# Optimization experiments

Hardware: AMD Instinct MI355X
Metric: run time of the kernel (lower is better)

## Reference

```python
import jax, jax.numpy as jnp
import numpy as np

B, S, H, R, F, E, K = 4, 2048, 1024, 256, 4096, 8, 2


def setup_inputs() -> dict:
    key = jax.random.key(0)
    k = jax.random.split(key, 7)
    s = 0.02
    return {
        "x": jax.random.normal(k[0], (B, S, H), dtype=jnp.float32),
        "router_w": jax.random.normal(k[1], (H, E), dtype=jnp.float32) * s,
        "router_b": jnp.zeros((E,), dtype=jnp.float32),
        "w1": jax.random.normal(k[2], (E, H, R), dtype=jnp.float32) * s,  # expert Linear(hidden->rank), no bias
        "w2": jax.random.normal(k[3], (E, R, F), dtype=jnp.float32) * s,  # expert Linear(rank->ffn), no bias
        "lin2_w": jax.random.normal(k[4], (F, H), dtype=jnp.float32) * s,
        "lin2_b": jnp.zeros((H,), dtype=jnp.float32),
    }


def reference(x, router_w, router_b, w1, w2, lin2_w, lin2_b):
    # Router: softmax over experts, top-k selection (mask), weight by softmax prob
    logits = jnp.einsum("bsh,he->bse", x, router_w) + router_b
    routing_weights = jax.nn.softmax(logits, axis=-1)            # [B,S,E]
    _, topk_idx = jax.lax.top_k(routing_weights, K)              # [B,S,K]
    mask = jnp.sum(jax.nn.one_hot(topk_idx, E, dtype=x.dtype), axis=-2)  # [B,S,E] in {0,1}
    mw = routing_weights * mask                                  # mask * weight per expert

    # Dense per-expert low-rank FFN (original computes all experts, masks after).
    # Fold mask*weight into the rank-space activations to avoid a [B,S,E,F] tensor.
    t = jnp.einsum("bsh,ehr->bser", x, w1)                       # [B,S,E,R]
    t = t * mw[..., None]
    mixed = jnp.einsum("bser,erf->bsf", t, w2)                   # [B,S,F]

    h = jax.nn.gelu(mixed, approximate=False)                    # torch nn.GELU is erf-based
    out = jnp.einsum("bsf,fh->bsh", h, lin2_w) + lin2_b
    # dropout is identity in eval mode
    return out
```

## Files before the change

kernel.cpp:

```cpp
#include <hip/hip_runtime.h>
#include <math.h>


using short8  = __attribute__((ext_vector_type(8))) short;
using floatx4 = __attribute__((ext_vector_type(4))) float;
typedef unsigned short bf16_t;

#define TOK   8192
#define HDIM  1024
#define RDIM  256
#define FDIM  4096
#define NEXP  8
#define MAXTILES 96
#define MAXSLOTS 16384

__device__ __forceinline__ bf16_t f2bf(float f) {
  union { float f; unsigned u; } a; a.f = f;
  unsigned u = a.u;
  return (bf16_t)((u + 0x7FFFu + ((u >> 16) & 1u)) >> 16);
}

__device__ __forceinline__ float gelu_erf(float v) {
  return 0.5f * v * (1.0f + erff(v * 0.70710678118654752f));
}

__device__ __forceinline__ void gload16(const void* g, void* l) {
  __builtin_amdgcn_global_load_lds(
      (const __attribute__((address_space(1))) void*)g,
      (__attribute__((address_space(3))) void*)l, 16, 0, 0);
}


__global__ void tcvt(const float* __restrict__ in, bf16_t* __restrict__ out,
                     int cols, size_t inSlice, size_t ldo,
                     int outRowStep, int outColStep) {
  __shared__ float tile[64][65];
  const int z  = blockIdx.z;
  const float* src = in + (size_t)z * inSlice;
  const int c0 = blockIdx.x * 64;
  const int r0 = blockIdx.y * 64;
  const int tx = threadIdx.x;
  const int ty = threadIdx.y;
#pragma unroll
  for (int i = 0; i < 64; i += 4)
    tile[ty + i][tx] = src[(size_t)(r0 + ty + i) * cols + (c0 + tx)];
  __syncthreads();
#pragma unroll
  for (int i = 0; i < 64; i += 4) {
    float v = tile[tx][ty + i];
    out[((size_t)(c0 + ty + i) + (size_t)z * outRowStep) * ldo +
        (size_t)z * outColStep + (r0 + tx)] = f2bf(v);
  }
}


__global__ void router_kernel(const float* __restrict__ x,
                              const float* __restrict__ rw,
                              const float* __restrict__ rb,
                              int* __restrict__ gid_tok,
                              float2* __restrict__ tokscale,
                              bf16_t* __restrict__ xb) {
  const int token = blockIdx.x * 4 + (threadIdx.x >> 6);
  const int lane  = threadIdx.x & 63;
  const float* xr = x + (size_t)token * HDIM;
  bf16_t* xbr = xb + (size_t)token * HDIM;

  double acc[NEXP];
#pragma unroll
  for (int e = 0; e < NEXP; e++) acc[e] = 0.0;
  for (int h = lane; h < HDIM; h += 64) {
    const float xf = xr[h];
    xbr[h] = f2bf(xf);
    const double xv = (double)xf;
    const float* wr = rw + (size_t)h * NEXP;
#pragma unroll
    for (int e = 0; e < NEXP; e++) acc[e] += xv * (double)wr[e];
  }
#pragma unroll
  for (int off = 32; off > 0; off >>= 1) {
#pragma unroll
    for (int e = 0; e < NEXP; e++) acc[e] += __shfl_xor(acc[e], off, 64);
  }
  double lg[NEXP];
#pragma unroll
  for (int e = 0; e < NEXP; e++) lg[e] = acc[e] + (double)rb[e];

  double mx = lg[0];
#pragma unroll
  for (int e = 1; e < NEXP; e++) mx = fmax(mx, lg[e]);
  double p[NEXP]; double den = 0.0;
#pragma unroll
  for (int e = 0; e < NEXP; e++) { p[e] = exp(lg[e] - mx); den += p[e]; }

  int i1 = 0;
#pragma unroll
  for (int e = 1; e < NEXP; e++) if (lg[e] > lg[i1]) i1 = e;
  int i2 = (i1 == 0) ? 1 : 0;
#pragma unroll
  for (int e = 0; e < NEXP; e++)
    if (e != i1 && e != i2 && lg[e] > lg[i2]) i2 = e;

  if (lane == 0) {
    const int elo = min(i1, i2), ehi = max(i1, i2);
    gid_tok[token] = elo * 8 + ehi;
    tokscale[token] = make_float2((float)(p[elo] / den), (float)(p[ehi] / den));
  }
}

__global__ void build_tiles(const int* __restrict__ gid_tok,
                            int* __restrict__ ctrl,
                            int* __restrict__ tok_of_slot,
                            float2* __restrict__ scale_of_slot) {
  __shared__ int hist[64], ntl[64];
  const int t = threadIdx.x;
  for (int i = t; i < MAXSLOTS; i += 256) {
    tok_of_slot[i] = -1;
    scale_of_slot[i] = make_float2(0.f, 0.f);
  }
  if (t < 64) { hist[t] = 0; }
  __syncthreads();
  for (int i = t; i < TOK; i += 256) atomicAdd(&hist[gid_tok[i]], 1);
  __syncthreads();
  if (t < 64) ntl[t] = (hist[t] + 127) >> 7;
  __syncthreads();
  if (t < 64) {
    int slot0 = 0, tile0 = 0;
    for (int g = 0; g < t; g++) { slot0 += ntl[g] << 7; tile0 += ntl[g]; }
    ctrl[64 + t] = 0;
    ctrl[128 + t] = slot0;
    const int nt = ntl[t], c = hist[t];
    for (int i = 0; i < nt; i++) {
      ctrl[256 + (tile0 + i) * 3 + 0] = t;
      ctrl[256 + (tile0 + i) * 3 + 1] = slot0 + i * 128;
      ctrl[256 + (tile0 + i) * 3 + 2] = min(128, c - i * 128);
    }
    if (t == 63) ctrl[192] = tile0 + nt;
  }
}

__global__ void scatter_tokens(const int* __restrict__ gid_tok,
                               const float2* __restrict__ tokscale,
                               int* __restrict__ ctrl,
                               int* __restrict__ tok_of_slot,
                               float2* __restrict__ scale_of_slot) {
  const int t = blockIdx.x * 256 + threadIdx.x;
  const int g = gid_tok[t];
  const int pos = atomicAdd(&ctrl[64 + g], 1);
  const int slot = ctrl[128 + g] + pos;
  tok_of_slot[slot] = t;
  scale_of_slot[slot] = tokscale[t];
}


__global__ __launch_bounds__(256)
void gemm_g1(const bf16_t* __restrict__ xb, const bf16_t* __restrict__ w1t,
             bf16_t* __restrict__ Tp, const int* __restrict__ ctrl,
             const int* __restrict__ tok_of_slot,
             const float2* __restrict__ scale_of_slot) {
  const int b = blockIdx.x;
  const int tile = b % MAXTILES, nt = b / MAXTILES;
  if (tile >= ctrl[192]) return;
  __shared__ bf16_t As[128 * 64];
  __shared__ bf16_t Bs[64 * 64];
  const int gid   = ctrl[256 + tile * 3];
  const int slot0 = ctrl[256 + tile * 3 + 1];
  const int e = (nt < 4) ? (gid >> 3) : (gid & 7);
  const int tid = threadIdx.x, lane = tid & 63, w = tid >> 6;
  const int l16 = lane & 15, quad = lane >> 4;
  const int rl = lane >> 3, gg = lane & 7;
  const int gf = (gg ^ rl) * 8;

  floatx4 acc[2][4];
  const floatx4 zero = {0.f, 0.f, 0.f, 0.f};
#pragma unroll
  for (int i = 0; i < 2; i++)
#pragma unroll
    for (int j = 0; j < 4; j++) acc[i][j] = zero;

  const bf16_t* ga[4];
#pragma unroll
  for (int c = 0; c < 4; c++) {
    int tk = tok_of_slot[slot0 + w * 32 + c * 8 + rl];
    if (tk < 0) tk = 0;
    ga[c] = xb + (size_t)tk * HDIM + gf;
  }
  const bf16_t* gb[2];
#pragma unroll
  for (int c = 0; c < 2; c++)
    gb[c] = w1t + (size_t)(e * 256 + (nt & 3) * 64 + w * 16 + c * 8 + rl) * HDIM + gf;
  bf16_t* lA = &As[w * 32 * 64];
  bf16_t* lB = &Bs[w * 16 * 64];

  for (int k0 = 0; k0 < HDIM; k0 += 64) {
    __syncthreads();
#pragma unroll
    for (int c = 0; c < 4; c++) { gload16(ga[c], lA + c * 512); ga[c] += 64; }
#pragma unroll
    for (int c = 0; c < 2; c++) { gload16(gb[c], lB + c * 512); gb[c] += 64; }
    __syncthreads();
#pragma unroll
    for (int s = 0; s < 2; s++) {
      const int pg = ((s * 4 + quad) ^ (l16 & 7)) * 8;
      short8 af[2], bfr[4];
#pragma unroll
      for (int i = 0; i < 2; i++)
        af[i] = *(const short8*)&As[(w * 32 + i * 16 + l16) * 64 + pg];
#pragma unroll
      for (int i = 0; i < 4; i++)
        bfr[i] = *(const short8*)&Bs[(i * 16 + l16) * 64 + pg];
#pragma unroll
      for (int mi = 0; mi < 2; mi++)
#pragma unroll
        for (int ni = 0; ni < 4; ni++)
          acc[mi][ni] = __builtin_amdgcn_mfma_f32_16x16x32_bf16(
              af[mi], bfr[ni], acc[mi][ni], 0, 0, 0);
    }
  }

#pragma unroll
  for (int mi = 0; mi < 2; mi++) {
#pragma unroll
    for (int r = 0; r < 4; r++) {
      const int srow = slot0 + w * 32 + mi * 16 + quad * 4 + r;
      const float2 sc = scale_of_slot[srow];
      const float s = (nt < 4) ? sc.x : sc.y;
#pragma unroll
      for (int ni = 0; ni < 4; ni++) {
        const int col = nt * 64 + ni * 16 + l16;
        Tp[(size_t)srow * 512 + col] = f2bf(acc[mi][ni][r] * s);
      }
    }
  }
}

__global__ __launch_bounds__(256)
void gemm_g2(const bf16_t* __restrict__ Tp, const bf16_t* __restrict__ w2t,
             bf16_t* __restrict__ Hb, const int* __restrict__ ctrl,
             const int* __restrict__ tok_of_slot) {
  const int b = blockIdx.x;
  const int tile = b % MAXTILES, n = b / MAXTILES;
  if (tile >= ctrl[192]) return;
  __shared__ bf16_t As[128 * 64];
  __shared__ bf16_t Bs[128 * 64];
  const int gid   = ctrl[256 + tile * 3];
  const int slot0 = ctrl[256 + tile * 3 + 1];
  const int n0 = n * 128;
  const int elo = gid >> 3, ehi = gid & 7;
  const int tid = threadIdx.x, lane = tid & 63, w = tid >> 6;
  const int wm = (w >> 1) * 64, wn = (w & 1) * 64;
  const int l16 = lane & 15, quad = lane >> 4;
  const int rl = lane >> 3, gg = lane & 7;
  const int gf = (gg ^ rl) * 8;

  floatx4 acc[4][4];
  const floatx4 zero = {0.f, 0.f, 0.f, 0.f};
#pragma unroll
  for (int i = 0; i < 4; i++)
#pragma unroll
    for (int j = 0; j < 4; j++) acc[i][j] = zero;

  const bf16_t* ga[4];
  const bf16_t* gbr[4];
#pragma unroll
  for (int c = 0; c < 4; c++) {
    ga[c]  = Tp + (size_t)(slot0 + w * 32 + c * 8 + rl) * 512 + gf;
    gbr[c] = w2t + (size_t)(n0 + w * 32 + c * 8 + rl) * 2048 + gf;
  }
  bf16_t* lA = &As[w * 32 * 64];
  bf16_t* lB = &Bs[w * 32 * 64];

#pragma unroll
  for (int t = 0; t < 8; t++) {
    const int e = (t < 4) ? elo : ehi;
    const int bcol = e * 256 + (t & 3) * 64;
    __syncthreads();
#pragma unroll
    for (int c = 0; c < 4; c++) { gload16(ga[c], lA + c * 512); ga[c] += 64; }
#pragma unroll
    for (int c = 0; c < 4; c++) gload16(gbr[c] + bcol, lB + c * 512);
    __syncthreads();
#pragma unroll
    for (int s = 0; s < 2; s++) {
      const int pg = ((s * 4 + quad) ^ (l16 & 7)) * 8;
      short8 af[4], bfr[4];
#pragma unroll
      for (int i = 0; i < 4; i++)
        af[i] = *(const short8*)&As[(wm + i * 16 + l16) * 64 + pg];
#pragma unroll
      for (int i = 0; i < 4; i++)
        bfr[i] = *(const short8*)&Bs[(wn + i * 16 + l16) * 64 + pg];
#pragma unroll
      for (int mi = 0; mi < 4; mi++)
#pragma unroll
        for (int ni = 0; ni < 4; ni++)
          acc[mi][ni] = __builtin_amdgcn_mfma_f32_16x16x32_bf16(
              af[mi], bfr[ni], acc[mi][ni], 0, 0, 0);
    }
  }

#pragma unroll
  for (int mi = 0; mi < 4; mi++) {
#pragma unroll
    for (int r = 0; r < 4; r++) {
      const int srow = slot0 + wm + mi * 16 + quad * 4 + r;
      const int tok = tok_of_slot[srow];
      if (tok < 0) continue;
#pragma unroll
      for (int ni = 0; ni < 4; ni++) {
        const int col = n0 + wn + ni * 16 + l16;
        Hb[(size_t)tok * FDIM + col] = f2bf(gelu_erf(acc[mi][ni][r]));
      }
    }
  }
}

__global__ __launch_bounds__(256)
void gemm_g3(const bf16_t* __restrict__ Hb, const bf16_t* __restrict__ ltw,
             float* __restrict__ out, const float* __restrict__ bias) {
  __shared__ bf16_t As[128 * 64];
  __shared__ bf16_t Bs[128 * 64];
  const int b = blockIdx.x;
  const int m0 = ((b & 7) * 8 + ((b >> 3) & 7)) * 128;
  const int n0 = (b >> 6) * 128;
  const int tid = threadIdx.x, lane = tid & 63, w = tid >> 6;
  const int wm = (w >> 1) * 64, wn = (w & 1) * 64;
  const int l16 = lane & 15, quad = lane >> 4;
  const int rl = lane >> 3, gg = lane & 7;
  const int gf = (gg ^ rl) * 8;

  floatx4 acc[4][4];
  const floatx4 zero = {0.f, 0.f, 0.f, 0.f};
#pragma unroll
  for (int i = 0; i < 4; i++)
#pragma unroll
    for (int j = 0; j < 4; j++) acc[i][j] = zero;

  const bf16_t* ga[4];
  const bf16_t* gb[4];
#pragma unroll
  for (int c = 0; c < 4; c++) {
    ga[c] = Hb  + (size_t)(m0 + w * 32 + c * 8 + rl) * FDIM + gf;
    gb[c] = ltw + (size_t)(n0 + w * 32 + c * 8 + rl) * FDIM + gf;
  }
  bf16_t* lA = &As[w * 32 * 64];
  bf16_t* lB = &Bs[w * 32 * 64];

  for (int k0 = 0; k0 < FDIM; k0 += 64) {
    __syncthreads();
#pragma unroll
    for (int c = 0; c < 4; c++) { gload16(ga[c], lA + c * 512); ga[c] += 64; }
#pragma unroll
    for (int c = 0; c < 4; c++) { gload16(gb[c], lB + c * 512); gb[c] += 64; }
    __syncthreads();
#pragma unroll
    for (int s = 0; s < 2; s++) {
      const int pg = ((s * 4 + quad) ^ (l16 & 7)) * 8;
      short8 af[4], bfr[4];
#pragma unroll
      for (int i = 0; i < 4; i++)
        af[i] = *(const short8*)&As[(wm + i * 16 + l16) * 64 + pg];
#pragma unroll
      for (int i = 0; i < 4; i++)
        bfr[i] = *(const short8*)&Bs[(wn + i * 16 + l16) * 64 + pg];
#pragma unroll
      for (int mi = 0; mi < 4; mi++)
#pragma unroll
        for (int ni = 0; ni < 4; ni++)
          acc[mi][ni] = __builtin_amdgcn_mfma_f32_16x16x32_bf16(
              af[mi], bfr[ni], acc[mi][ni], 0, 0, 0);
    }
  }

#pragma unroll
  for (int mi = 0; mi < 4; mi++) {
#pragma unroll
    for (int ni = 0; ni < 4; ni++) {
      const int row = m0 + wm + mi * 16 + quad * 4;
      const int col = n0 + wn + ni * 16 + l16;
#pragma unroll
      for (int r = 0; r < 4; r++)
        out[(size_t)(row + r) * HDIM + col] = acc[mi][ni][r] + bias[col];
    }
  }
}


extern "C" void kernel_launch(void* const* d_in, const int* in_sizes, int n_in,
                              void* d_out, int out_size, void* d_ws, size_t ws_size,
                              hipStream_t stream) {
  const float* x   = (const float*)d_in[0];
  const float* rw  = (const float*)d_in[1];
  const float* rb  = (const float*)d_in[2];
  const float* w1  = (const float*)d_in[3];
  const float* w2  = (const float*)d_in[4];
  const float* l2w = (const float*)d_in[5];
  const float* l2b = (const float*)d_in[6];

  char* ws = (char*)d_ws;
  int*    ctrl     = (int*)   (ws + 0);
  int*    gid_tok  = (int*)   (ws + 4096);
  float2* tokscale = (float2*)(ws + 36864);
  int*    tokslot  = (int*)   (ws + 102400);
  float2* slotsc   = (float2*)(ws + 167936);
  bf16_t* xb  = (bf16_t*)(ws + 1048576);
  bf16_t* w1t = (bf16_t*)(ws + 17825792);
  bf16_t* w2t = (bf16_t*)(ws + 22020096);
  bf16_t* ltw = (bf16_t*)(ws + 38797312);
  bf16_t* Tp  = (bf16_t*)(ws + 47185920);
  bf16_t* Hb  = (bf16_t*)(ws + 63963136);

  router_kernel<<<TOK / 4, 256, 0, stream>>>(x, rw, rb, gid_tok, tokscale, xb);
  build_tiles<<<1, 256, 0, stream>>>(gid_tok, ctrl, tokslot, slotsc);
  scatter_tokens<<<TOK / 256, 256, 0, stream>>>(gid_tok, tokscale, ctrl, tokslot, slotsc);

  tcvt<<<dim3(RDIM / 64, HDIM / 64, NEXP), dim3(64, 4), 0, stream>>>(
      w1, w1t, RDIM, (size_t)HDIM * RDIM, HDIM, RDIM, 0);
  tcvt<<<dim3(FDIM / 64, RDIM / 64, NEXP), dim3(64, 4), 0, stream>>>(
      w2, w2t, FDIM, (size_t)RDIM * FDIM, 2048, 0, RDIM);
  tcvt<<<dim3(HDIM / 64, FDIM / 64, 1), dim3(64, 4), 0, stream>>>(
      l2w, ltw, HDIM, 0, FDIM, 0, 0);

  gemm_g1<<<8 * MAXTILES, 256, 0, stream>>>(xb, w1t, Tp, ctrl, tokslot, slotsc);
  gemm_g2<<<32 * MAXTILES, 256, 0, stream>>>(Tp, w2t, Hb, ctrl, tokslot);
  gemm_g3<<<512, 256, 0, stream>>>(Hb, ltw, (float*)d_out, l2b);
}
```

Before: 366.2 us.

## Pre-pack operands into swizzled 128x128 bf16 tile images with K=128 stages

Replaces the transpose-convert kernels with pack kernels that write weights as contiguous, pre-swizzled 128x128 bf16 tile images. The intermediate activations (Tp, Hb) are also written directly in this tiled image layout. All three GEMMs then load whole tiles with fully contiguous 16-byte global-to-LDS copies and use K=128 per stage, halving the barrier count. gemm_g1 moves to 128x128 output tiles with fewer blocks. The cost is doubled LDS per block (64 KB), which may lower occupancy, plus more complex scattered epilogue writes into the tiled images.

```diff
diff --git a/kernel.cpp b/kernel.cpp
--- a/kernel.cpp
+++ b/kernel.cpp
@@ -13,6 +13,7 @@
 #define NEXP  8
 #define MAXTILES 96
 #define MAXSLOTS 16384
+#define IMG   16384
 
 __device__ __forceinline__ bf16_t f2bf(float f) {
   union { float f; unsigned u; } a; a.f = f;
@@ -30,27 +31,43 @@
       (__attribute__((address_space(3))) void*)l, 16, 0, 0);
 }
 
-
-__global__ void tcvt(const float* __restrict__ in, bf16_t* __restrict__ out,
-                     int cols, size_t inSlice, size_t ldo,
-                     int outRowStep, int outColStep) {
-  __shared__ float tile[64][65];
-  const int z  = blockIdx.z;
-  const float* src = in + (size_t)z * inSlice;
-  const int c0 = blockIdx.x * 64;
-  const int r0 = blockIdx.y * 64;
-  const int tx = threadIdx.x;
-  const int ty = threadIdx.y;
-#pragma unroll
-  for (int i = 0; i < 64; i += 4)
-    tile[ty + i][tx] = src[(size_t)(r0 + ty + i) * cols + (c0 + tx)];
+__device__ __forceinline__ int swz_off(int r, int kl) {
+  return r * 128 + ((((kl >> 3) ^ (r & 15)) << 3) | (kl & 7));
+}
+
+
+__device__ __forceinline__ void pack_tile_body(const float* __restrict__ src,
+                                               size_t kStride,
+                                               bf16_t* __restrict__ img) {
+  __shared__ bf16_t lim[IMG];
+  const int tid = threadIdx.x;
+  const int rr = tid & 127, half = tid >> 7;
+  for (int kl = half; kl < 128; kl += 2)
+    lim[swz_off(rr, kl)] = f2bf(src[(size_t)kl * kStride + rr]);
   __syncthreads();
-#pragma unroll
-  for (int i = 0; i < 64; i += 4) {
-    float v = tile[tx][ty + i];
-    out[((size_t)(c0 + ty + i) + (size_t)z * outRowStep) * ldo +
-        (size_t)z * outColStep + (r0 + tx)] = f2bf(v);
-  }
+  const int4* s4 = (const int4*)lim;
+  int4* d4 = (int4*)img;
+#pragma unroll
+  for (int i = 0; i < 8; i++) d4[tid + i * 256] = s4[tid + i * 256];
+}
+
+__global__ void pack_w1(const float* __restrict__ w1, bf16_t* __restrict__ w1p) {
+  const int img = blockIdx.x;
+  const int e = img >> 4, nc = (img >> 3) & 1, kb = img & 7;
+  pack_tile_body(w1 + (size_t)e * 1024 * 256 + (size_t)kb * 128 * 256 + nc * 128,
+                 256, w1p + (size_t)img * IMG);
+}
+__global__ void pack_w2(const float* __restrict__ w2, bf16_t* __restrict__ w2p) {
+  const int img = blockIdx.x;
+  const int n = img >> 4, e = (img >> 1) & 7, kb = img & 1;
+  pack_tile_body(w2 + (size_t)e * 256 * 4096 + (size_t)kb * 128 * 4096 + n * 128,
+                 4096, w2p + (size_t)img * IMG);
+}
+__global__ void pack_ltw(const float* __restrict__ l2w, bf16_t* __restrict__ ltwp) {
+  const int img = blockIdx.x;
+  const int n = img >> 5, kb = img & 31;
+  pack_tile_body(l2w + (size_t)kb * 128 * 1024 + n * 128, 1024,
+                 ltwp + (size_t)img * IMG);
 }
 
 
@@ -117,7 +134,7 @@
     tok_of_slot[i] = -1;
     scale_of_slot[i] = make_float2(0.f, 0.f);
   }
-  if (t < 64) { hist[t] = 0; }
+  if (t < 64) hist[t] = 0;
   __syncthreads();
   for (int i = t; i < TOK; i += 256) atomicAdd(&hist[gid_tok[i]], 1);
   __syncthreads();
@@ -153,63 +170,60 @@
 
 
 __global__ __launch_bounds__(256)
-void gemm_g1(const bf16_t* __restrict__ xb, const bf16_t* __restrict__ w1t,
+void gemm_g1(const bf16_t* __restrict__ xb, const bf16_t* __restrict__ w1p,
              bf16_t* __restrict__ Tp, const int* __restrict__ ctrl,
              const int* __restrict__ tok_of_slot,
              const float2* __restrict__ scale_of_slot) {
   const int b = blockIdx.x;
-  const int tile = b % MAXTILES, nt = b / MAXTILES;
+  const int tile = b >> 2, nt = b & 3;
   if (tile >= ctrl[192]) return;
-  __shared__ bf16_t As[128 * 64];
-  __shared__ bf16_t Bs[64 * 64];
+  __shared__ bf16_t As[IMG];
+  __shared__ bf16_t Bs[IMG];
   const int gid   = ctrl[256 + tile * 3];
   const int slot0 = ctrl[256 + tile * 3 + 1];
-  const int e = (nt < 4) ? (gid >> 3) : (gid & 7);
+  const int e = (nt < 2) ? (gid >> 3) : (gid & 7);
+  const int nc = nt & 1;
   const int tid = threadIdx.x, lane = tid & 63, w = tid >> 6;
+  const int wm = (w >> 1) * 64, wn = (w & 1) * 64;
   const int l16 = lane & 15, quad = lane >> 4;
-  const int rl = lane >> 3, gg = lane & 7;
-  const int gf = (gg ^ rl) * 8;
-
-  floatx4 acc[2][4];
+
+  floatx4 acc[4][4];
   const floatx4 zero = {0.f, 0.f, 0.f, 0.f};
 #pragma unroll
-  for (int i = 0; i < 2; i++)
+  for (int i = 0; i < 4; i++)
 #pragma unroll
     for (int j = 0; j < 4; j++) acc[i][j] = zero;
 
-  const bf16_t* ga[4];
-#pragma unroll
-  for (int c = 0; c < 4; c++) {
-    int tk = tok_of_slot[slot0 + w * 32 + c * 8 + rl];
-    if (tk < 0) tk = 0;
-    ga[c] = xb + (size_t)tk * HDIM + gf;
-  }
-  const bf16_t* gb[2];
-#pragma unroll
-  for (int c = 0; c < 2; c++)
-    gb[c] = w1t + (size_t)(e * 256 + (nt & 3) * 64 + w * 16 + c * 8 + rl) * HDIM + gf;
-  bf16_t* lA = &As[w * 32 * 64];
-  bf16_t* lB = &Bs[w * 16 * 64];
-
-  for (int k0 = 0; k0 < HDIM; k0 += 64) {
-    __syncthreads();
-#pragma unroll
-    for (int c = 0; c < 4; c++) { gload16(ga[c], lA + c * 512); ga[c] += 64; }
-#pragma unroll
-    for (int c = 0; c < 2; c++) { gload16(gb[c], lB + c * 512); gb[c] += 64; }
-    __syncthreads();
-#pragma unroll
-    for (int s = 0; s < 2; s++) {
-      const int pg = ((s * 4 + quad) ^ (l16 & 7)) * 8;
-      short8 af[2], bfr[4];
-#pragma unroll
-      for (int i = 0; i < 2; i++)
-        af[i] = *(const short8*)&As[(w * 32 + i * 16 + l16) * 64 + pg];
-#pragma unroll
-      for (int i = 0; i < 4; i++)
-        bfr[i] = *(const short8*)&Bs[(i * 16 + l16) * 64 + pg];
-#pragma unroll
-      for (int mi = 0; mi < 2; mi++)
+  int toks[8];
+#pragma unroll
+  for (int i = 0; i < 8; i++) {
+    int tk = tok_of_slot[slot0 + w * 32 + i * 4 + (lane >> 4)];
+    toks[i] = (tk < 0) ? 0 : tk;
+  }
+  const bf16_t* bimg = w1p + (size_t)(e * 16 + nc * 8) * IMG;
+  bf16_t* lA = As + w * 4096;
+  bf16_t* lB = Bs + w * 4096;
+
+  for (int kb = 0; kb < 8; kb++) {
+    __syncthreads();
+#pragma unroll
+    for (int i = 0; i < 8; i++) {
+      const int g = (lane & 15) ^ ((i * 4 + (lane >> 4)) & 15);
+      gload16(xb + (size_t)toks[i] * HDIM + kb * 128 + g * 8, lA + i * 512);
+      gload16(bimg + (size_t)kb * IMG + w * 4096 + i * 512 + lane * 8, lB + i * 512);
+    }
+    __syncthreads();
+#pragma unroll
+    for (int s = 0; s < 4; s++) {
+      const int pg = ((s * 4 + quad) ^ l16) << 3;
+      short8 af[4], bfr[4];
+#pragma unroll
+      for (int i = 0; i < 4; i++) {
+        af[i]  = *(const short8*)&As[(wm + i * 16 + l16) * 128 + pg];
+        bfr[i] = *(const short8*)&Bs[(wn + i * 16 + l16) * 128 + pg];
+      }
+#pragma unroll
+      for (int mi = 0; mi < 4; mi++)
 #pragma unroll
         for (int ni = 0; ni < 4; ni++)
           acc[mi][ni] = __builtin_amdgcn_mfma_f32_16x16x32_bf16(
@@ -217,40 +231,38 @@
     }
   }
 
-#pragma unroll
-  for (int mi = 0; mi < 2; mi++) {
+  bf16_t* img = Tp + (size_t)(tile * 4 + nt) * IMG;
+#pragma unroll
+  for (int mi = 0; mi < 4; mi++) {
 #pragma unroll
     for (int r = 0; r < 4; r++) {
-      const int srow = slot0 + w * 32 + mi * 16 + quad * 4 + r;
-      const float2 sc = scale_of_slot[srow];
-      const float s = (nt < 4) ? sc.x : sc.y;
+      const int rl = wm + mi * 16 + quad * 4 + r;
+      const float2 sc = scale_of_slot[slot0 + rl];
+      const float s = (nt < 2) ? sc.x : sc.y;
 #pragma unroll
       for (int ni = 0; ni < 4; ni++) {
-        const int col = nt * 64 + ni * 16 + l16;
-        Tp[(size_t)srow * 512 + col] = f2bf(acc[mi][ni][r] * s);
+        const int c = wn + ni * 16 + l16;
+        img[swz_off(rl, c)] = f2bf(acc[mi][ni][r] * s);
       }
     }
   }
 }
 
 __global__ __launch_bounds__(256)
-void gemm_g2(const bf16_t* __restrict__ Tp, const bf16_t* __restrict__ w2t,
-             bf16_t* __restrict__ Hb, const int* __restrict__ ctrl,
+void gemm_g2(const bf16_t* __restrict__ Tp, const bf16_t* __restrict__ w2p,
+             bf16_t* __restrict__ Hbp, const int* __restrict__ ctrl,
              const int* __restrict__ tok_of_slot) {
   const int b = blockIdx.x;
-  const int tile = b % MAXTILES, n = b / MAXTILES;
+  const int tile = b >> 5, n = b & 31;
   if (tile >= ctrl[192]) return;
-  __shared__ bf16_t As[128 * 64];
-  __shared__ bf16_t Bs[128 * 64];
+  __shared__ bf16_t As[IMG];
+  __shared__ bf16_t Bs[IMG];
   const int gid   = ctrl[256 + tile * 3];
   const int slot0 = ctrl[256 + tile * 3 + 1];
-  const int n0 = n * 128;
   const int elo = gid >> 3, ehi = gid & 7;
   const int tid = threadIdx.x, lane = tid & 63, w = tid >> 6;
   const int wm = (w >> 1) * 64, wn = (w & 1) * 64;
   const int l16 = lane & 15, quad = lane >> 4;
-  const int rl = lane >> 3, gg = lane & 7;
-  const int gf = (gg ^ rl) * 8;
 
   floatx4 acc[4][4];
   const floatx4 zero = {0.f, 0.f, 0.f, 0.f};
@@ -259,36 +271,30 @@
 #pragma unroll
     for (int j = 0; j < 4; j++) acc[i][j] = zero;
 
-  const bf16_t* ga[4];
-  const bf16_t* gbr[4];
-#pragma unroll
-  for (int c = 0; c < 4; c++) {
-    ga[c]  = Tp + (size_t)(slot0 + w * 32 + c * 8 + rl) * 512 + gf;
-    gbr[c] = w2t + (size_t)(n0 + w * 32 + c * 8 + rl) * 2048 + gf;
-  }
-  bf16_t* lA = &As[w * 32 * 64];
-  bf16_t* lB = &Bs[w * 32 * 64];
-
-#pragma unroll
-  for (int t = 0; t < 8; t++) {
-    const int e = (t < 4) ? elo : ehi;
-    const int bcol = e * 256 + (t & 3) * 64;
-    __syncthreads();
-#pragma unroll
-    for (int c = 0; c < 4; c++) { gload16(ga[c], lA + c * 512); ga[c] += 64; }
-#pragma unroll
-    for (int c = 0; c < 4; c++) gload16(gbr[c] + bcol, lB + c * 512);
-    __syncthreads();
-#pragma unroll
-    for (int s = 0; s < 2; s++) {
-      const int pg = ((s * 4 + quad) ^ (l16 & 7)) * 8;
+  const bf16_t* aimg = Tp + (size_t)tile * 4 * IMG;
+  bf16_t* lA = As + w * 4096;
+  bf16_t* lB = Bs + w * 4096;
+
+#pragma unroll
+  for (int t = 0; t < 4; t++) {
+    const int e = (t < 2) ? elo : ehi;
+    const bf16_t* bimg = w2p + (size_t)(n * 16 + e * 2 + (t & 1)) * IMG;
+    __syncthreads();
+#pragma unroll
+    for (int i = 0; i < 8; i++) {
+      gload16(aimg + (size_t)t * IMG + w * 4096 + i * 512 + lane * 8, lA + i * 512);
+      gload16(bimg + w * 4096 + i * 512 + lane * 8, lB + i * 512);
+    }
+    __syncthreads();
+#pragma unroll
+    for (int s = 0; s < 4; s++) {
+      const int pg = ((s * 4 + quad) ^ l16) << 3;
       short8 af[4], bfr[4];
 #pragma unroll
-      for (int i = 0; i < 4; i++)
-        af[i] = *(const short8*)&As[(wm + i * 16 + l16) * 64 + pg];
-#pragma unroll
-      for (int i = 0; i < 4; i++)
-        bfr[i] = *(const short8*)&Bs[(wn + i * 16 + l16) * 64 + pg];
+      for (int i = 0; i < 4; i++) {
+        af[i]  = *(const short8*)&As[(wm + i * 16 + l16) * 128 + pg];
+        bfr[i] = *(const short8*)&Bs[(wn + i * 16 + l16) * 128 + pg];
+      }
 #pragma unroll
       for (int mi = 0; mi < 4; mi++)
 #pragma unroll
@@ -305,28 +311,28 @@
       const int srow = slot0 + wm + mi * 16 + quad * 4 + r;
       const int tok = tok_of_slot[srow];
       if (tok < 0) continue;
+      bf16_t* img = Hbp + (size_t)((tok >> 7) * 32 + n) * IMG;
+      const int rloc = tok & 127;
 #pragma unroll
       for (int ni = 0; ni < 4; ni++) {
-        const int col = n0 + wn + ni * 16 + l16;
-        Hb[(size_t)tok * FDIM + col] = f2bf(gelu_erf(acc[mi][ni][r]));
+        const int kl = wn + ni * 16 + l16;
+        img[swz_off(rloc, kl)] = f2bf(gelu_erf(acc[mi][ni][r]));
       }
     }
   }
 }
 
 __global__ __launch_bounds__(256)
-void gemm_g3(const bf16_t* __restrict__ Hb, const bf16_t* __restrict__ ltw,
+void gemm_g3(const bf16_t* __restrict__ Hbp, const bf16_t* __restrict__ ltwp,
              float* __restrict__ out, const float* __restrict__ bias) {
-  __shared__ bf16_t As[128 * 64];
-  __shared__ bf16_t Bs[128 * 64];
+  __shared__ bf16_t As[IMG];
+  __shared__ bf16_t Bs[IMG];
   const int b = blockIdx.x;
-  const int m0 = ((b & 7) * 8 + ((b >> 3) & 7)) * 128;
-  const int n0 = (b >> 6) * 128;
+  const int mtile = (b & 7) * 8 + ((b >> 3) & 7);
+  const int n = b >> 6;
   const int tid = threadIdx.x, lane = tid & 63, w = tid >> 6;
   const int wm = (w >> 1) * 64, wn = (w & 1) * 64;
   const int l16 = lane & 15, quad = lane >> 4;
-  const int rl = lane >> 3, gg = lane & 7;
-  const int gf = (gg ^ rl) * 8;
 
   floatx4 acc[4][4];
   const floatx4 zero = {0.f, 0.f, 0.f, 0.f};
@@ -335,33 +341,28 @@
 #pragma unroll
     for (int j = 0; j < 4; j++) acc[i][j] = zero;
 
-  const bf16_t* ga[4];
-  const bf16_t* gb[4];
-#pragma unroll
-  for (int c = 0; c < 4; c++) {
-    ga[c] = Hb  + (size_t)(m0 + w * 32 + c * 8 + rl) * FDIM + gf;
-    gb[c] = ltw + (size_t)(n0 + w * 32 + c * 8 + rl) * FDIM + gf;
-  }
-  bf16_t* lA = &As[w * 32 * 64];
-  bf16_t* lB = &Bs[w * 32 * 64];
-
-  for (int k0 = 0; k0 < FDIM; k0 += 64) {
-    __syncthreads();
-#pragma unroll
-    for (int c = 0; c < 4; c++) { gload16(ga[c], lA + c * 512); ga[c] += 64; }
-#pragma unroll
-    for (int c = 0; c < 4; c++) { gload16(gb[c], lB + c * 512); gb[c] += 64; }
-    __syncthreads();
-#pragma unroll
-    for (int s = 0; s < 2; s++) {
-      const int pg = ((s * 4 + quad) ^ (l16 & 7)) * 8;
+  const bf16_t* aimg = Hbp + (size_t)mtile * 32 * IMG;
+  const bf16_t* bimg = ltwp + (size_t)n * 32 * IMG;
+  bf16_t* lA = As + w * 4096;
+  bf16_t* lB = Bs + w * 4096;
+
+  for (int kb = 0; kb < 32; kb++) {
+    __syncthreads();
+#pragma unroll
+    for (int i = 0; i < 8; i++) {
+      gload16(aimg + (size_t)kb * IMG + w * 4096 + i * 512 + lane * 8, lA + i * 512);
+      gload16(bimg + (size_t)kb * IMG + w * 4096 + i * 512 + lane * 8, lB + i * 512);
+    }
+    __syncthreads();
+#pragma unroll
+    for (int s = 0; s < 4; s++) {
+      const int pg = ((s * 4 + quad) ^ l16) << 3;
       short8 af[4], bfr[4];
 #pragma unroll
-      for (int i = 0; i < 4; i++)
-        af[i] = *(const short8*)&As[(wm + i * 16 + l16) * 64 + pg];
-#pragma unroll
-      for (int i = 0; i < 4; i++)
-        bfr[i] = *(const short8*)&Bs[(wn + i * 16 + l16) * 64 + pg];
+      for (int i = 0; i < 4; i++) {
+        af[i]  = *(const short8*)&As[(wm + i * 16 + l16) * 128 + pg];
+        bfr[i] = *(const short8*)&Bs[(wn + i * 16 + l16) * 128 + pg];
+      }
 #pragma unroll
       for (int mi = 0; mi < 4; mi++)
 #pragma unroll
@@ -375,8 +376,8 @@
   for (int mi = 0; mi < 4; mi++) {
 #pragma unroll
     for (int ni = 0; ni < 4; ni++) {
-      const int row = m0 + wm + mi * 16 + quad * 4;
-      const int col = n0 + wn + ni * 16 + l16;
+      const int row = mtile * 128 + wm + mi * 16 + quad * 4;
+      const int col = n * 128 + wn + ni * 16 + l16;
 #pragma unroll
       for (int r = 0; r < 4; r++)
         out[(size_t)(row + r) * HDIM + col] = acc[mi][ni][r] + bias[col];
@@ -402,25 +403,22 @@
   float2* tokscale = (float2*)(ws + 36864);
   int*    tokslot  = (int*)   (ws + 102400);
   float2* slotsc   = (float2*)(ws + 167936);
-  bf16_t* xb  = (bf16_t*)(ws + 1048576);
-  bf16_t* w1t = (bf16_t*)(ws + 17825792);
-  bf16_t* w2t = (bf16_t*)(ws + 22020096);
-  bf16_t* ltw = (bf16_t*)(ws + 38797312);
-  bf16_t* Tp  = (bf16_t*)(ws + 47185920);
-  bf16_t* Hb  = (bf16_t*)(ws + 63963136);
+  bf16_t* xb   = (bf16_t*)(ws + 1048576);
+  bf16_t* w1p  = (bf16_t*)(ws + 17825792);
+  bf16_t* w2p  = (bf16_t*)(ws + 22020096);
+  bf16_t* ltwp = (bf16_t*)(ws + 38797312);
+  bf16_t* Tp   = (bf16_t*)(ws + 47185920);
+  bf16_t* Hbp  = (bf16_t*)(ws + 59768832);
 
   router_kernel<<<TOK / 4, 256, 0, stream>>>(x, rw, rb, gid_tok, tokscale, xb);
   build_tiles<<<1, 256, 0, stream>>>(gid_tok, ctrl, tokslot, slotsc);
   scatter_tokens<<<TOK / 256, 256, 0, stream>>>(gid_tok, tokscale, ctrl, tokslot, slotsc);
 
-  tcvt<<<dim3(RDIM / 64, HDIM / 64, NEXP), dim3(64, 4), 0, stream>>>(
-      w1, w1t, RDIM, (size_t)HDIM * RDIM, HDIM, RDIM, 0);
-  tcvt<<<dim3(FDIM / 64, RDIM / 64, NEXP), dim3(64, 4), 0, stream>>>(
-      w2, w2t, FDIM, (size_t)RDIM * FDIM, 2048, 0, RDIM);
-  tcvt<<<dim3(HDIM / 64, FDIM / 64, 1), dim3(64, 4), 0, stream>>>(
-      l2w, ltw, HDIM, 0, FDIM, 0, 0);
-
-  gemm_g1<<<8 * MAXTILES, 256, 0, stream>>>(xb, w1t, Tp, ctrl, tokslot, slotsc);
-  gemm_g2<<<32 * MAXTILES, 256, 0, stream>>>(Tp, w2t, Hb, ctrl, tokslot);
-  gemm_g3<<<512, 256, 0, stream>>>(Hb, ltw, (float*)d_out, l2b);
-}
+  pack_w1<<<128, 256, 0, stream>>>(w1, w1p);
+  pack_w2<<<512, 256, 0, stream>>>(w2, w2p);
+  pack_ltw<<<256, 256, 0, stream>>>(l2w, ltwp);
+
+  gemm_g1<<<4 * MAXTILES, 256, 0, stream>>>(xb, w1p, Tp, ctrl, tokslot, slotsc);
+  gemm_g2<<<32 * MAXTILES, 256, 0, stream>>>(Tp, w2p, Hbp, ctrl, tokslot);
+  gemm_g3<<<512, 256, 0, stream>>>(Hbp, ltwp, (float*)d_out, l2b);
+}
```

Result: slower. 375.6 us (+2.5%).

## Pre-pack expert weights into swizzled tile images and restructure expert GEMMs

Applied to the files above, without the earlier changes.

Replaces the w1/w2 transpose-convert with pack kernels that write each 128x128 bf16 weight block as a pre-swizzled contiguous image, so the grouped GEMMs can stream B tiles with plain linear loads. gemm_g1 and gemm_g2 now use 64-row M halves with K=128 steps, skip the second half when a tile holds 64 rows or fewer, and stage outputs through LDS. g1 writes the intermediate in the same tiled image layout for g2, and g2 writes full 16-byte rows into the scattered token positions. The risks are doubled block counts for g2, extra LDS traffic in the epilogue, and less reuse per block from the smaller M tiles.

```diff
diff --git a/kernel.cpp b/kernel.cpp
--- a/kernel.cpp
+++ b/kernel.cpp
@@ -13,6 +13,7 @@
 #define NEXP  8
 #define MAXTILES 96
 #define MAXSLOTS 16384
+#define IMG   16384
 
 __device__ __forceinline__ bf16_t f2bf(float f) {
   union { float f; unsigned u; } a; a.f = f;
@@ -30,6 +31,38 @@
       (__attribute__((address_space(3))) void*)l, 16, 0, 0);
 }
 
+__device__ __forceinline__ int swz_off(int r, int kl) {
+  return r * 128 + ((((kl >> 3) ^ (r & 15)) << 3) | (kl & 7));
+}
+
+
+__device__ __forceinline__ void pack_tile_body(const float* __restrict__ src,
+                                               size_t kStride,
+                                               bf16_t* __restrict__ img) {
+  __shared__ bf16_t lim[IMG];
+  const int tid = threadIdx.x;
+  const int rr = tid & 127, half = tid >> 7;
+  for (int kl = half; kl < 128; kl += 2)
+    lim[swz_off(rr, kl)] = f2bf(src[(size_t)kl * kStride + rr]);
+  __syncthreads();
+  const int4* s4 = (const int4*)lim;
+  int4* d4 = (int4*)img;
+#pragma unroll
+  for (int i = 0; i < 8; i++) d4[tid + i * 256] = s4[tid + i * 256];
+}
+
+__global__ void pack_w1(const float* __restrict__ w1, bf16_t* __restrict__ w1p) {
+  const int img = blockIdx.x;
+  const int e = img >> 4, nc = (img >> 3) & 1, kb = img & 7;
+  pack_tile_body(w1 + (size_t)e * 1024 * 256 + (size_t)kb * 128 * 256 + nc * 128,
+                 256, w1p + (size_t)img * IMG);
+}
+__global__ void pack_w2(const float* __restrict__ w2, bf16_t* __restrict__ w2p) {
+  const int img = blockIdx.x;
+  const int n = img >> 4, e = (img >> 1) & 7, kb = img & 1;
+  pack_tile_body(w2 + (size_t)e * 256 * 4096 + (size_t)kb * 128 * 4096 + n * 128,
+                 4096, w2p + (size_t)img * IMG);
+}
 
 __global__ void tcvt(const float* __restrict__ in, bf16_t* __restrict__ out,
                      int cols, size_t inSlice, size_t ldo,
@@ -117,7 +150,7 @@
     tok_of_slot[i] = -1;
     scale_of_slot[i] = make_float2(0.f, 0.f);
   }
-  if (t < 64) { hist[t] = 0; }
+  if (t < 64) hist[t] = 0;
   __syncthreads();
   for (int i = t; i < TOK; i += 256) atomicAdd(&hist[gid_tok[i]], 1);
   __syncthreads();
@@ -151,24 +184,25 @@
   scale_of_slot[slot] = tokscale[t];
 }
 
-
 __global__ __launch_bounds__(256)
-void gemm_g1(const bf16_t* __restrict__ xb, const bf16_t* __restrict__ w1t,
+void gemm_g1(const bf16_t* __restrict__ xb, const bf16_t* __restrict__ w1p,
              bf16_t* __restrict__ Tp, const int* __restrict__ ctrl,
              const int* __restrict__ tok_of_slot,
              const float2* __restrict__ scale_of_slot) {
   const int b = blockIdx.x;
-  const int tile = b % MAXTILES, nt = b / MAXTILES;
+  const int tile = b >> 3, mh = (b >> 2) & 1, n = b & 3;
   if (tile >= ctrl[192]) return;
-  __shared__ bf16_t As[128 * 64];
-  __shared__ bf16_t Bs[64 * 64];
+  const int nrows = ctrl[256 + tile * 3 + 2];
+  if (mh && nrows <= 64) return;
+  __shared__ bf16_t As[64 * 128];
+  __shared__ bf16_t Bs[128 * 128];
   const int gid   = ctrl[256 + tile * 3];
   const int slot0 = ctrl[256 + tile * 3 + 1];
-  const int e = (nt < 4) ? (gid >> 3) : (gid & 7);
+  const int e = (n < 2) ? (gid >> 3) : (gid & 7);
+  const int nc = n & 1;
   const int tid = threadIdx.x, lane = tid & 63, w = tid >> 6;
+  const int wm = (w & 1) * 32, wn = (w >> 1) * 64;
   const int l16 = lane & 15, quad = lane >> 4;
-  const int rl = lane >> 3, gg = lane & 7;
-  const int gf = (gg ^ rl) * 8;
 
   floatx4 acc[2][4];
   const floatx4 zero = {0.f, 0.f, 0.f, 0.f};
@@ -177,37 +211,39 @@
 #pragma unroll
     for (int j = 0; j < 4; j++) acc[i][j] = zero;
 
-  const bf16_t* ga[4];
-#pragma unroll
-  for (int c = 0; c < 4; c++) {
-    int tk = tok_of_slot[slot0 + w * 32 + c * 8 + rl];
-    if (tk < 0) tk = 0;
-    ga[c] = xb + (size_t)tk * HDIM + gf;
-  }
-  const bf16_t* gb[2];
-#pragma unroll
-  for (int c = 0; c < 2; c++)
-    gb[c] = w1t + (size_t)(e * 256 + (nt & 3) * 64 + w * 16 + c * 8 + rl) * HDIM + gf;
-  bf16_t* lA = &As[w * 32 * 64];
-  bf16_t* lB = &Bs[w * 16 * 64];
-
-  for (int k0 = 0; k0 < HDIM; k0 += 64) {
-    __syncthreads();
-#pragma unroll
-    for (int c = 0; c < 4; c++) { gload16(ga[c], lA + c * 512); ga[c] += 64; }
-#pragma unroll
-    for (int c = 0; c < 2; c++) { gload16(gb[c], lB + c * 512); gb[c] += 64; }
-    __syncthreads();
-#pragma unroll
-    for (int s = 0; s < 2; s++) {
-      const int pg = ((s * 4 + quad) ^ (l16 & 7)) * 8;
+  int toks[4];
+  int rowAs[4];
+#pragma unroll
+  for (int i = 0; i < 4; i++) {
+    rowAs[i] = w * 16 + i * 4 + (lane >> 4);
+    int tk = tok_of_slot[slot0 + mh * 64 + rowAs[i]];
+    toks[i] = (tk < 0) ? 0 : tk;
+  }
+  const bf16_t* bimg = w1p + (size_t)(e * 16 + nc * 8) * IMG;
+  bf16_t* lA = As + w * 2048;
+  bf16_t* lB = Bs + w * 4096;
+
+  for (int kb = 0; kb < 8; kb++) {
+    __syncthreads();
+#pragma unroll
+    for (int i = 0; i < 4; i++) {
+      const int gq = (lane & 15) ^ (rowAs[i] & 15);
+      gload16(xb + (size_t)toks[i] * HDIM + kb * 128 + gq * 8, lA + i * 512);
+    }
+#pragma unroll
+    for (int i = 0; i < 8; i++)
+      gload16(bimg + (size_t)kb * IMG + w * 4096 + i * 512 + lane * 8, lB + i * 512);
+    __syncthreads();
+#pragma unroll
+    for (int s = 0; s < 4; s++) {
+      const int pg = ((s * 4 + quad) ^ l16) << 3;
       short8 af[2], bfr[4];
 #pragma unroll
       for (int i = 0; i < 2; i++)
-        af[i] = *(const short8*)&As[(w * 32 + i * 16 + l16) * 64 + pg];
+        af[i] = *(const short8*)&As[(wm + i * 16 + l16) * 128 + pg];
 #pragma unroll
       for (int i = 0; i < 4; i++)
-        bfr[i] = *(const short8*)&Bs[(i * 16 + l16) * 64 + pg];
+        bfr[i] = *(const short8*)&Bs[(wn + i * 16 + l16) * 128 + pg];
 #pragma unroll
       for (int mi = 0; mi < 2; mi++)
 #pragma unroll
@@ -217,80 +253,82 @@
     }
   }
 
+  __syncthreads();
 #pragma unroll
   for (int mi = 0; mi < 2; mi++) {
 #pragma unroll
     for (int r = 0; r < 4; r++) {
-      const int srow = slot0 + w * 32 + mi * 16 + quad * 4 + r;
-      const float2 sc = scale_of_slot[srow];
-      const float s = (nt < 4) ? sc.x : sc.y;
+      const int rloc = wm + mi * 16 + quad * 4 + r;
+      const float2 sc = scale_of_slot[slot0 + mh * 64 + rloc];
+      const float s = (n < 2) ? sc.x : sc.y;
 #pragma unroll
       for (int ni = 0; ni < 4; ni++) {
-        const int col = nt * 64 + ni * 16 + l16;
-        Tp[(size_t)srow * 512 + col] = f2bf(acc[mi][ni][r] * s);
+        const int c = wn + ni * 16 + l16;
+        As[swz_off(rloc, c)] = f2bf(acc[mi][ni][r] * s);
       }
     }
   }
+  __syncthreads();
+  bf16_t* img = Tp + (size_t)(tile * 4 + n) * IMG + mh * 64 * 128;
+  const int4* s4 = (const int4*)As;
+  int4* d4 = (int4*)img;
+#pragma unroll
+  for (int j = 0; j < 4; j++) d4[tid + j * 256] = s4[tid + j * 256];
 }
 
 __global__ __launch_bounds__(256)
-void gemm_g2(const bf16_t* __restrict__ Tp, const bf16_t* __restrict__ w2t,
+void gemm_g2(const bf16_t* __restrict__ Tp, const bf16_t* __restrict__ w2p,
              bf16_t* __restrict__ Hb, const int* __restrict__ ctrl,
              const int* __restrict__ tok_of_slot) {
   const int b = blockIdx.x;
-  const int tile = b % MAXTILES, n = b / MAXTILES;
+  const int tile = b >> 6, mh = (b >> 5) & 1, n = b & 31;
   if (tile >= ctrl[192]) return;
-  __shared__ bf16_t As[128 * 64];
-  __shared__ bf16_t Bs[128 * 64];
+  const int nrows = ctrl[256 + tile * 3 + 2];
+  if (mh && nrows <= 64) return;
+  __shared__ bf16_t As[64 * 128];
+  __shared__ bf16_t Bs[128 * 128];
   const int gid   = ctrl[256 + tile * 3];
   const int slot0 = ctrl[256 + tile * 3 + 1];
-  const int n0 = n * 128;
   const int elo = gid >> 3, ehi = gid & 7;
   const int tid = threadIdx.x, lane = tid & 63, w = tid >> 6;
-  const int wm = (w >> 1) * 64, wn = (w & 1) * 64;
+  const int wm = (w & 1) * 32, wn = (w >> 1) * 64;
   const int l16 = lane & 15, quad = lane >> 4;
-  const int rl = lane >> 3, gg = lane & 7;
-  const int gf = (gg ^ rl) * 8;
-
-  floatx4 acc[4][4];
+
+  floatx4 acc[2][4];
   const floatx4 zero = {0.f, 0.f, 0.f, 0.f};
 #pragma unroll
-  for (int i = 0; i < 4; i++)
+  for (int i = 0; i < 2; i++)
 #pragma unroll
     for (int j = 0; j < 4; j++) acc[i][j] = zero;
 
-  const bf16_t* ga[4];
-  const bf16_t* gbr[4];
-#pragma unroll
-  for (int c = 0; c < 4; c++) {
-    ga[c]  = Tp + (size_t)(slot0 + w * 32 + c * 8 + rl) * 512 + gf;
-    gbr[c] = w2t + (size_t)(n0 + w * 32 + c * 8 + rl) * 2048 + gf;
-  }
-  bf16_t* lA = &As[w * 32 * 64];
-  bf16_t* lB = &Bs[w * 32 * 64];
-
-#pragma unroll
-  for (int t = 0; t < 8; t++) {
-    const int e = (t < 4) ? elo : ehi;
-    const int bcol = e * 256 + (t & 3) * 64;
-    __syncthreads();
-#pragma unroll
-    for (int c = 0; c < 4; c++) { gload16(ga[c], lA + c * 512); ga[c] += 64; }
-#pragma unroll
-    for (int c = 0; c < 4; c++) gload16(gbr[c] + bcol, lB + c * 512);
-    __syncthreads();
-#pragma unroll
-    for (int s = 0; s < 2; s++) {
-      const int pg = ((s * 4 + quad) ^ (l16 & 7)) * 8;
-      short8 af[4], bfr[4];
+  const bf16_t* aimg = Tp + (size_t)tile * 4 * IMG + mh * 64 * 128;
+  bf16_t* lA = As + w * 2048;
+  bf16_t* lB = Bs + w * 4096;
+
+#pragma unroll
+  for (int t = 0; t < 4; t++) {
+    const int e = (t < 2) ? elo : ehi;
+    const bf16_t* bimg = w2p + (size_t)(n * 16 + e * 2 + (t & 1)) * IMG;
+    __syncthreads();
+#pragma unroll
+    for (int i = 0; i < 4; i++)
+      gload16(aimg + (size_t)t * IMG + w * 2048 + i * 512 + lane * 8, lA + i * 512);
+#pragma unroll
+    for (int i = 0; i < 8; i++)
+      gload16(bimg + w * 4096 + i * 512 + lane * 8, lB + i * 512);
+    __syncthreads();
+#pragma unroll
+    for (int s = 0; s < 4; s++) {
+      const int pg = ((s * 4 + quad) ^ l16) << 3;
+      short8 af[2], bfr[4];
+#pragma unroll
+      for (int i = 0; i < 2; i++)
+        af[i] = *(const short8*)&As[(wm + i * 16 + l16) * 128 + pg];
 #pragma unroll
       for (int i = 0; i < 4; i++)
-        af[i] = *(const short8*)&As[(wm + i * 16 + l16) * 64 + pg];
-#pragma unroll
-      for (int i = 0; i < 4; i++)
-        bfr[i] = *(const short8*)&Bs[(wn + i * 16 + l16) * 64 + pg];
-#pragma unroll
-      for (int mi = 0; mi < 4; mi++)
+        bfr[i] = *(const short8*)&Bs[(wn + i * 16 + l16) * 128 + pg];
+#pragma unroll
+      for (int mi = 0; mi < 2; mi++)
 #pragma unroll
         for (int ni = 0; ni < 4; ni++)
           acc[mi][ni] = __builtin_amdgcn_mfma_f32_16x16x32_bf16(
@@ -298,19 +336,28 @@
     }
   }
 
-#pragma unroll
-  for (int mi = 0; mi < 4; mi++) {
+  __syncthreads();
+#pragma unroll
+  for (int mi = 0; mi < 2; mi++) {
 #pragma unroll
     for (int r = 0; r < 4; r++) {
-      const int srow = slot0 + wm + mi * 16 + quad * 4 + r;
-      const int tok = tok_of_slot[srow];
-      if (tok < 0) continue;
+      const int rloc = wm + mi * 16 + quad * 4 + r;
 #pragma unroll
       for (int ni = 0; ni < 4; ni++) {
-        const int col = n0 + wn + ni * 16 + l16;
-        Hb[(size_t)tok * FDIM + col] = f2bf(gelu_erf(acc[mi][ni][r]));
+        const int c = wn + ni * 16 + l16;
+        Bs[rloc * 128 + c] = f2bf(gelu_erf(acc[mi][ni][r]));
       }
     }
+  }
+  __syncthreads();
+  const int4* s4 = (const int4*)Bs;
+#pragma unroll
+  for (int j = 0; j < 4; j++) {
+    const int chunk = tid + j * 256;
+    const int row = chunk >> 4, off = chunk & 15;
+    const int tok = tok_of_slot[slot0 + mh * 64 + row];
+    if (tok >= 0)
+      *(int4*)(Hb + (size_t)tok * FDIM + n * 128 + off * 8) = s4[chunk];
   }
 }
 
@@ -403,24 +450,22 @@
   int*    tokslot  = (int*)   (ws + 102400);
   float2* slotsc   = (float2*)(ws + 167936);
   bf16_t* xb  = (bf16_t*)(ws + 1048576);
-  bf16_t* w1t = (bf16_t*)(ws + 17825792);
-  bf16_t* w2t = (bf16_t*)(ws + 22020096);
+  bf16_t* w1p = (bf16_t*)(ws + 17825792);
+  bf16_t* w2p = (bf16_t*)(ws + 22020096);
   bf16_t* ltw = (bf16_t*)(ws + 38797312);
   bf16_t* Tp  = (bf16_t*)(ws + 47185920);
-  bf16_t* Hb  = (bf16_t*)(ws + 63963136);
+  bf16_t* Hb  = (bf16_t*)(ws + 59768832);
 
   router_kernel<<<TOK / 4, 256, 0, stream>>>(x, rw, rb, gid_tok, tokscale, xb);
   build_tiles<<<1, 256, 0, stream>>>(gid_tok, ctrl, tokslot, slotsc);
   scatter_tokens<<<TOK / 256, 256, 0, stream>>>(gid_tok, tokscale, ctrl, tokslot, slotsc);
 
-  tcvt<<<dim3(RDIM / 64, HDIM / 64, NEXP), dim3(64, 4), 0, stream>>>(
-      w1, w1t, RDIM, (size_t)HDIM * RDIM, HDIM, RDIM, 0);
-  tcvt<<<dim3(FDIM / 64, RDIM / 64, NEXP), dim3(64, 4), 0, stream>>>(
-      w2, w2t, FDIM, (size_t)RDIM * FDIM, 2048, 0, RDIM);
+  pack_w1<<<128, 256, 0, stream>>>(w1, w1p);
+  pack_w2<<<512, 256, 0, stream>>>(w2, w2p);
   tcvt<<<dim3(HDIM / 64, FDIM / 64, 1), dim3(64, 4), 0, stream>>>(
       l2w, ltw, HDIM, 0, FDIM, 0, 0);
 
-  gemm_g1<<<8 * MAXTILES, 256, 0, stream>>>(xb, w1t, Tp, ctrl, tokslot, slotsc);
-  gemm_g2<<<32 * MAXTILES, 256, 0, stream>>>(Tp, w2t, Hb, ctrl, tokslot);
+  gemm_g1<<<8 * MAXTILES, 256, 0, stream>>>(xb, w1p, Tp, ctrl, tokslot, slotsc);
+  gemm_g2<<<64 * MAXTILES, 256, 0, stream>>>(Tp, w2p, Hb, ctrl, tokslot);
   gemm_g3<<<512, 256, 0, stream>>>(Hb, ltw, (float*)d_out, l2b);
 }
```

New measurement: 354.1 us. -3.3%, faster.
